# Optimization experiments

Measured on AMD Instinct MI355X. Metric: run time of the kernel, lower is better.

## Reference

```python
import jax, jax.numpy as jnp
import numpy as np

B, N, K = 4, 16384, 8
NF = [8, 32, 64, 128, 256]
E = N * K


def setup_inputs() -> dict:
    key = jax.random.key(0)
    ks = jax.random.split(key, 16)
    x = jax.random.normal(ks[0], (B, N, NF[0]), jnp.float32)
    # knn-style edge list: every node appears as a center K times (no empty segments)
    centers = jnp.tile(jnp.repeat(jnp.arange(N), K)[None, None, :], (B, 1, 1))
    neighbors = jax.random.randint(ks[1], (B, 1, E), 0, N)
    edge_index = jnp.concatenate([centers, neighbors], axis=1)
    specs = [("0a", NF[0], NF[1]), ("0b", NF[0], NF[1]),
             ("1a", NF[1], NF[2]), ("1b", NF[1], NF[2]),
             ("2a", NF[2], NF[3]), ("2b", NF[2], NF[3]),
             ("3a", NF[3], NF[4]), ("3b", NF[3], NF[4]),
             ("cat", NF[1] + NF[2] + NF[3] + NF[4], 1)]
    inp = {"x": x, "edge_index": edge_index}
    for i, (nm, ci, co) in enumerate(specs):
        inp["W" + nm] = jax.random.normal(ks[2 + i], (ci, co), jnp.float32) / np.sqrt(ci)
        inp["g" + nm] = jnp.ones((co,), jnp.float32)   # BN gamma
        inp["b" + nm] = jnp.zeros((co,), jnp.float32)  # BN beta
    inp["bias"] = jnp.zeros((1,), jnp.float32)
    return inp


def _bn(x, g, b):
    # training-mode BatchNorm1d over all rows (GraphBatchNorm1d reduces over batch*num_points)
    m = x.mean(0)
    v = jnp.mean(jnp.square(x - m), 0)  # biased variance, as torch BN uses for normalization
    return g * (x - m) * jax.lax.rsqrt(v + 1e-5) + b


def _mlp(x, W, g, b):
    # Linear(bias=False) -> BN -> LeakyReLU(0.2)
    return jax.nn.leaky_relu(_bn(x @ W, g, b), negative_slope=0.2)


def reference(x, edge_index,
              W0a, g0a, b0a, W0b, g0b, b0b,
              W1a, g1a, b1a, W1b, g1b, b1b,
              W2a, g2a, b2a, W2b, g2b, b2b,
              W3a, g3a, b3a, W3b, g3b, b3b,
              Wcat, gcat, bcat, bias):
    BN = B * N
    xf = x.reshape(BN, NF[0])
    ei = edge_index.transpose(1, 0, 2).reshape(2, -1)  # [2, B*E]
    off = jnp.repeat(jnp.arange(B) * N, E)
    centers = ei[0] + off
    neighbors = ei[1] + off
    segmax = lambda v: jax.ops.segment_max(v, centers, num_segments=BN)
    x0 = _mlp(xf, W0a, g0a, b0a) + segmax(_mlp(xf[neighbors] - xf[centers], W0b, g0b, b0b))
    x1 = _mlp(x0, W1a, g1a, b1a) + segmax(_mlp(x0, W1b, g1b, b1b)[neighbors])
    x2 = _mlp(x1, W2a, g2a, b2a) + segmax(_mlp(x1, W2b, g2b, b2b)[neighbors])
    x3 = _mlp(x2, W3a, g3a, b3a) + segmax(_mlp(x2, W3b, g3b, b3b)[neighbors])
    x_cat = _mlp(jnp.concatenate([x0, x1, x2, x3], axis=-1), Wcat, gcat, bcat)
    return x_cat + bias
```

## Files before the change

kernel.cpp:

```cpp
#include <hip/hip_runtime.h>
#include <math.h>

static constexpr int BB = 4;
static constexpr int NN = 16384;
static constexpr int KK = 8;
static constexpr int EE = 131072;
static constexpr int RR = 65536;
static constexpr int EG = 524288;

static constexpr int SPL = 64;
static constexpr size_t SLOT = (size_t)SPL*512;

static constexpr size_t OFF_X0 = 0;
static constexpr size_t OFF_X1 = OFF_X0 + (size_t)RR*32;
static constexpr size_t OFF_X2 = OFF_X1 + (size_t)RR*64;
static constexpr size_t OFF_X3 = OFF_X2 + (size_t)RR*128;
static constexpr size_t OFF_ZB = OFF_X3 + (size_t)RR*256;
static constexpr size_t OFF_ZC = OFF_ZB + (size_t)RR*128;
static constexpr size_t OFF_S  = OFF_ZC + (size_t)RR;
static constexpr size_t OFF_WP = OFF_S + 9*SLOT;
static constexpr size_t WP1_OFF = 0;
static constexpr size_t WP2_OFF = 4096;
static constexpr size_t WP3_OFF = 4096 + 16384;

__device__ __forceinline__ float lrelu(float x) { return fmaxf(x, 0.2f*x); }

__device__ __forceinline__ unsigned short f2h(float f) {
    _Float16 h = (_Float16)f;
    return *(unsigned short*)&h;
}
__device__ __forceinline__ float h2f(unsigned short u) {
    _Float16 h = *(_Float16*)&u;
    return (float)h;
}

typedef __attribute__((ext_vector_type(8))) _Float16 half8v;
typedef __attribute__((ext_vector_type(8))) unsigned short ushort8v;
typedef __attribute__((ext_vector_type(4))) float float4v;

__global__ __launch_bounds__(256) void k_l0_node(const float* __restrict__ xf,
                                                 const float* __restrict__ W,
                                                 unsigned short* __restrict__ z,
                                                 float* __restrict__ S) {
    __shared__ float w[256];
    __shared__ float red[64];
    int tid = threadIdx.x;
    w[tid] = W[tid];
    if (tid < 64) red[tid] = 0.f;
    __syncthreads();
    int r = blockIdx.x*256 + tid;
    const float4* xr = (const float4*)(xf + (size_t)r*8);
    float4 a = xr[0], b = xr[1];
    float xv[8] = {a.x,a.y,a.z,a.w,b.x,b.y,b.z,b.w};
    float op[32];
#pragma unroll
    for (int c = 0; c < 32; ++c) {
        float s = 0.f;
#pragma unroll
        for (int k = 0; k < 8; ++k) s = fmaf(xv[k], w[k*32+c], s);
        op[c] = s;
    }
    ushort8v* zp = (ushort8v*)(z + (size_t)r*32);
#pragma unroll
    for (int i = 0; i < 4; ++i) {
        ushort8v h;
#pragma unroll
        for (int j = 0; j < 8; ++j) h[j] = f2h(op[i*8+j]);
        zp[i] = h;
    }
#pragma unroll
    for (int c = 0; c < 32; ++c) {
        float s = op[c], q = op[c]*op[c];
#pragma unroll
        for (int off = 32; off >= 1; off >>= 1) {
            s += __shfl_xor(s, off, 64);
            q += __shfl_xor(q, off, 64);
        }
        if ((tid & 63) == 0) { atomicAdd(&red[c], s); atomicAdd(&red[32+c], q); }
    }
    __syncthreads();
    if (tid < 64) atomicAdd(&S[(size_t)(blockIdx.x & (SPL-1))*512 + tid], red[tid]);
}

__global__ __launch_bounds__(256) void k_edge_stats(const float* __restrict__ xf,
                                                    const int* __restrict__ ei,
                                                    const float* __restrict__ W,
                                                    float* __restrict__ S) {
    __shared__ float w[256];
    __shared__ float red[64];
    int tid = threadIdx.x;
    w[tid] = W[tid];
    if (tid < 64) red[tid] = 0.f;
    __syncthreads();
    int g = tid & 3;
    int cg = g*8;
    float s[8], q[8];
#pragma unroll
    for (int j = 0; j < 8; ++j) { s[j] = 0.f; q[j] = 0.f; }
    int qid = (blockIdx.x*256 + tid) >> 2;
    int NQ = (gridDim.x*256) >> 2;
    for (int e = qid; e < EG; e += NQ) {
        int b = e >> 17, jj = e & (EE-1);
        const int* base = ei + (size_t)b*2*EE;
        int ctr = base[jj], nbr = base[EE + jj];
        const float4* pc = (const float4*)(xf + ((size_t)(b<<14) + ctr)*8);
        const float4* pn = (const float4*)(xf + ((size_t)(b<<14) + nbr)*8);
        float4 c0 = pc[0], c1 = pc[1], n0 = pn[0], n1 = pn[1];
        float d[8] = {n0.x-c0.x, n0.y-c0.y, n0.z-c0.z, n0.w-c0.w,
                      n1.x-c1.x, n1.y-c1.y, n1.z-c1.z, n1.w-c1.w};
#pragma unroll
        for (int j = 0; j < 8; ++j) {
            int c = cg + j;
            float z = 0.f;
#pragma unroll
            for (int k = 0; k < 8; ++k) z = fmaf(d[k], w[k*32+c], z);
            s[j] += z; q[j] = fmaf(z, z, q[j]);
        }
    }
#pragma unroll
    for (int off = 4; off <= 32; off <<= 1) {
#pragma unroll
        for (int j = 0; j < 8; ++j) {
            s[j] += __shfl_xor(s[j], off, 64);
            q[j] += __shfl_xor(q[j], off, 64);
        }
    }
    if ((tid & 63) < 4) {
#pragma unroll
        for (int j = 0; j < 8; ++j) {
            atomicAdd(&red[cg + j], s[j]);
            atomicAdd(&red[32 + cg + j], q[j]);
        }
    }
    __syncthreads();
    if (tid < 64) atomicAdd(&S[(size_t)(blockIdx.x & (SPL-1))*512 + tid], red[tid]);
}

__global__ __launch_bounds__(256) void k_edge_apply(const float* __restrict__ xf,
                                                    const int* __restrict__ ei,
                                                    const float* __restrict__ W,
                                                    const float* __restrict__ Sa,
                                                    const float* __restrict__ Sb,
                                                    const float* __restrict__ ga,
                                                    const float* __restrict__ ba,
                                                    const float* __restrict__ gb,
                                                    const float* __restrict__ bbp,
                                                    const float* __restrict__ Wc,
                                                    unsigned short* __restrict__ x0,
                                                    float* __restrict__ zc) {
    __shared__ float w[256];
    __shared__ float scb[32], shb[32], sca[32], sha[32], swc[32];
    int tid = threadIdx.x;
    w[tid] = W[tid];
    if (tid < 32) {
        float su = 0.f, qu = 0.f;
        for (int p = 0; p < SPL; ++p) { su += Sa[(size_t)p*512 + tid]; qu += Sa[(size_t)p*512 + 32 + tid]; }
        float m = su*(1.f/RR);
        float v = fmaxf(qu*(1.f/RR) - m*m, 0.f);
        float sc = ga[tid]*rsqrtf(v + 1e-5f);
        sca[tid] = sc; sha[tid] = fmaf(-m, sc, ba[tid]);
        swc[tid] = Wc[tid];
    } else if (tid < 64) {
        int c = tid - 32;
        float su = 0.f, qu = 0.f;
        for (int p = 0; p < SPL; ++p) { su += Sb[(size_t)p*512 + c]; qu += Sb[(size_t)p*512 + 32 + c]; }
        float m = su*(1.f/EG);
        float v = fmaxf(qu*(1.f/EG) - m*m, 0.f);
        float sc = gb[c]*rsqrtf(v + 1e-5f);
        scb[c] = sc; shb[c] = fmaf(-m, sc, bbp[c]);
    }
    __syncthreads();
    int r = blockIdx.x*256 + tid;
    int b = r >> 14, n = r & (NN-1);
    const int* nb = ei + (size_t)b*2*EE + EE + n*KK;
    const float4* pc = (const float4*)(xf + (size_t)r*8);
    float4 c0 = pc[0], c1 = pc[1];
    float mx[32];
#pragma unroll
    for (int c = 0; c < 32; ++c) mx[c] = -3.0e38f;
    for (int k = 0; k < KK; ++k) {
        int j = nb[k];
        const float4* pn = (const float4*)(xf + ((size_t)(b<<14) + j)*8);
        float4 n0 = pn[0], n1 = pn[1];
        float d[8] = {n0.x-c0.x, n0.y-c0.y, n0.z-c0.z, n0.w-c0.w,
                      n1.x-c1.x, n1.y-c1.y, n1.z-c1.z, n1.w-c1.w};
#pragma unroll
        for (int c = 0; c < 32; ++c) {
            float z = 0.f;
#pragma unroll
            for (int k2 = 0; k2 < 8; ++k2) z = fmaf(d[k2], w[k2*32+c], z);
            float y = lrelu(fmaf(z, scb[c], shb[c]));
            mx[c] = fmaxf(mx[c], y);
        }
    }
    ushort8v* xp = (ushort8v*)(x0 + (size_t)r*32);
    float sdot = 0.f;
#pragma unroll
    for (int i = 0; i < 4; ++i) {
        ushort8v v = xp[i];
        ushort8v o;
#pragma unroll
        for (int j = 0; j < 8; ++j) {
            int c = i*8 + j;
            float val = lrelu(fmaf(h2f(v[j]), sca[c], sha[c])) + mx[c];
            o[j] = f2h(val);
            sdot = fmaf(val, swc[c], sdot);
        }
        xp[i] = o;
    }
    zc[r] = sdot;
}

template<int CI, int CO>
__global__ __launch_bounds__(256) void k_packW(const float* __restrict__ Wa,
                                               const float* __restrict__ Wb,
                                               unsigned short* __restrict__ Wp) {
    constexpr int NT = 2*CO;
    constexpr int KT = CI/32;
    int t = blockIdx.x*256 + threadIdx.x;
    if (t >= NT*CI) return;
    int ng = t % NT, k = t / NT;
    float v = (ng < CO) ? Wa[(size_t)k*CO + ng] : Wb[(size_t)k*CO + (ng - CO)];
    int nt = ng >> 4, n = ng & 15;
    int kt = k >> 5, kq = (k & 31) >> 3, j = k & 7;
    int f = nt*KT + kt;
    int idx = f*512 + ((kq*16 + n)<<3) + j;
    Wp[idx] = f2h(v);
}

template<int CI, int CO>
__global__ __launch_bounds__(256, 3) void k_mfma_dual3(const unsigned short* __restrict__ X,
                                                       const unsigned short* __restrict__ Wp,
                                                       unsigned short* __restrict__ Za,
                                                       unsigned short* __restrict__ Zb,
                                                       float* __restrict__ Sa,
                                                       float* __restrict__ Sb) {
    constexpr int NCH = 4;
    constexpr int KT = CI/32;
    constexpr int WCNT = NCH*KT*512;
    constexpr int ROWT = RR/64;
    constexpr int STR = NCH*16 + 8;
    constexpr int XW  = (CI < 64) ? CI : 64;
    constexpr int PLB = CO/64;
    __shared__ unsigned short Wlds[WCNT];
    __shared__ unsigned short scr[4][16*STR];
    int tid = threadIdx.x;
    int lane = tid & 63, wid = tid >> 6;
    int ch = blockIdx.y;
    int wglob = blockIdx.x*4 + wid;
    int NW = gridDim.x*4;
    int n = lane & 15, kq = lane >> 4;
    int rg = lane >> 3, c8l = (lane & 7)*8;
    unsigned short* myscr = scr[wid];
    size_t pl = (size_t)(wglob & (SPL-1)) * 512;
    bool isA = (ch < PLB);
    unsigned short* Zp = (isA ? Za : Zb) + (size_t)(isA ? ch : ch - PLB)*((size_t)RR*64);
    {
        const ushort8v* src = (const ushort8v*)(Wp + (size_t)ch*WCNT);
        ushort8v* dst = (ushort8v*)Wlds;
        for (int u = tid; u < WCNT/8; u += 256) dst[u] = src[u];
    }
    __syncthreads();

    float4v ps[NCH], pq[NCH];
#pragma unroll
    for (int j = 0; j < NCH; ++j) { ps[j] = (float4v){0,0,0,0}; pq[j] = (float4v){0,0,0,0}; }

    auto issue = [&](half8v (&dst)[4], size_t rowb, int kt) {
        int k0 = kt*32 + kq*8;
        int xpl = k0 >> 6;
        int xoff = k0 & (XW-1);
        const unsigned short* Xp = X + (size_t)xpl*((size_t)RR*64);
#pragma unroll
        for (int i = 0; i < 4; ++i)
            dst[i] = *(const half8v*)&Xp[(rowb + i*16 + n)*XW + xoff];
    };

    auto epilogue = [&](float4v (&acc)[4][NCH], size_t rowbase) {
#pragma unroll
        for (int j = 0; j < NCH; ++j)
#pragma unroll
            for (int i = 0; i < 4; ++i) {
                float4v a4 = acc[i][j];
#pragma unroll
                for (int reg = 0; reg < 4; ++reg) {
                    ps[j][reg] += a4[reg];
                    pq[j][reg] = fmaf(a4[reg], a4[reg], pq[j][reg]);
                }
            }
#pragma unroll
        for (int i = 0; i < 4; ++i) {
            __builtin_amdgcn_wave_barrier();
#pragma unroll
            for (int j = 0; j < NCH; ++j) {
                float4v a4 = acc[i][j];
                ushort4 h = { f2h(a4[0]), f2h(a4[1]), f2h(a4[2]), f2h(a4[3]) };
                *(ushort4*)&myscr[n*STR + j*16 + kq*4] = h;
            }
            __builtin_amdgcn_wave_barrier();
#pragma unroll
            for (int i2 = 0; i2 < 2; ++i2) {
                int rit = rg + i2*8;
                ushort8v v = *(const ushort8v*)&myscr[rit*STR + c8l];
                *(ushort8v*)&Zp[(rowbase + i*16 + rit)*64 + c8l] = v;
            }
        }
    };

    if constexpr (KT == 1) {
        for (int t = wglob; t < ROWT; t += NW) {
            size_t rowbase = (size_t)t*64;
            float4v acc[4][NCH];
#pragma unroll
            for (int i = 0; i < 4; ++i)
#pragma unroll
                for (int j = 0; j < NCH; ++j) acc[i][j] = (float4v){0,0,0,0};
            half8v b[4];
            issue(b, rowbase, 0);
#pragma unroll
            for (int j = 0; j < NCH; ++j) {
                half8v w = *(const half8v*)&Wlds[j*512 + lane*8];
#pragma unroll
                for (int i = 0; i < 4; ++i)
                    acc[i][j] = __builtin_amdgcn_mfma_f32_16x16x32_f16(w, b[i], acc[i][j], 0, 0, 0);
            }
            epilogue(acc, rowbase);
        }
    } else {
        half8v b0[4], b1[4];
        int t = wglob;
        if (t < ROWT) issue(b0, (size_t)t*64, 0);
        for (; t < ROWT; t += NW) {
            size_t rowbase = (size_t)t*64;
            int t2 = t + NW;
            size_t nextrb = (t2 < ROWT) ? (size_t)t2*64 : rowbase;
            float4v acc[4][NCH];
#pragma unroll
            for (int i = 0; i < 4; ++i)
#pragma unroll
                for (int j = 0; j < NCH; ++j) acc[i][j] = (float4v){0,0,0,0};

            auto step = [&](half8v (&bc)[4], half8v (&bn)[4], int kt) {
                if (kt + 1 < KT) issue(bn, rowbase, kt + 1);
                else             issue(bn, nextrb, 0);
#pragma unroll
                for (int j = 0; j < NCH; ++j) {
                    half8v w = *(const half8v*)&Wlds[(j*KT + kt)*512 + lane*8];
#pragma unroll
                    for (int i = 0; i < 4; ++i)
                        acc[i][j] = __builtin_amdgcn_mfma_f32_16x16x32_f16(w, bc[i], acc[i][j], 0, 0, 0);
                }
            };
#pragma unroll
            for (int kh = 0; kh < KT/2; ++kh) {
                step(b0, b1, 2*kh);
                step(b1, b0, 2*kh + 1);
            }
            epilogue(acc, rowbase);
        }
    }

    {
        float* Sg = isA ? Sa : Sb;
        int cb0 = isA ? ch*64 : ch*64 - CO;
#pragma unroll
        for (int j = 0; j < NCH; ++j) {
#pragma unroll
            for (int reg = 0; reg < 4; ++reg) {
                float s = ps[j][reg], q = pq[j][reg];
                s += __shfl_xor(s, 1, 64); q += __shfl_xor(q, 1, 64);
                s += __shfl_xor(s, 2, 64); q += __shfl_xor(q, 2, 64);
                s += __shfl_xor(s, 4, 64); q += __shfl_xor(q, 4, 64);
                s += __shfl_xor(s, 8, 64); q += __shfl_xor(q, 8, 64);
                if (n == 0) {
                    int col = cb0 + j*16 + kq*4 + reg;
                    atomicAdd(&Sg[pl + col], s);
                    atomicAdd(&Sg[pl + CO + col], q);
                }
            }
        }
    }
}

template<int CO>
__global__ __launch_bounds__(256) void k_redstats(float* __restrict__ Sa,
                                                  float* __restrict__ Sb) {
    int t = blockIdx.x*256 + threadIdx.x;
    for (int u = t; u < 2*CO; u += gridDim.x*256) {
        float sa = 0.f, sb = 0.f;
        for (int p = 1; p < SPL; ++p) {
            sa += Sa[(size_t)p*512 + u];
            sb += Sb[(size_t)p*512 + u];
        }
        Sa[u] += sa;
        Sb[u] += sb;
    }
}

template<int CO, bool WRITEBACK>
__global__ __launch_bounds__(256) void k_gathermax(unsigned short* __restrict__ xi,
                                                   const unsigned short* __restrict__ zbh,
                                                   const int* __restrict__ ei,
                                                   const float* __restrict__ Sa,
                                                   const float* __restrict__ Sb,
                                                   const float* __restrict__ ga,
                                                   const float* __restrict__ ba,
                                                   const float* __restrict__ gb,
                                                   const float* __restrict__ bbp,
                                                   const float* __restrict__ Wc,
                                                   int wcoff,
                                                   float* __restrict__ zc) {
    constexpr int CQ = CO/8;
    __shared__ float sca[CO], sha[CO], scb[CO], shb[CO], swc[CO];
    int tid = threadIdx.x;
    for (int u = tid; u < CO; u += 256) {
        float m = Sa[u]*(1.f/RR);
        float v = fmaxf(Sa[CO+u]*(1.f/RR) - m*m, 0.f);
        float sc = ga[u]*rsqrtf(v + 1e-5f);
        sca[u] = sc; sha[u] = fmaf(-m, sc, ba[u]);
        m = Sb[u]*(1.f/RR);
        v = fmaxf(Sb[CO+u]*(1.f/RR) - m*m, 0.f);
        sc = gb[u]*rsqrtf(v + 1e-5f);
        scb[u] = sc; shb[u] = fmaf(-m, sc, bbp[u]);
        swc[u] = Wc[wcoff + u];
    }
    __syncthreads();
    int t = blockIdx.x*256 + tid;
    int r = t / CQ;
    int c8 = (t % CQ)*8;
    int pln = c8 >> 6;
    int off = c8 & 63;
    const unsigned short* zpl = zbh + (size_t)pln*((size_t)RR*64);
    unsigned short* xpl = xi + (size_t)pln*((size_t)RR*64);
    int b = r >> 14, n = r & (NN-1);
    const int* nb = ei + (size_t)b*2*EE + EE + n*KK;
    float sb[8], hb[8];
#pragma unroll
    for (int j = 0; j < 8; ++j) { sb[j] = scb[c8+j]; hb[j] = shb[c8+j]; }
    int nbr[KK];
#pragma unroll
    for (int k = 0; k < KK; ++k) nbr[k] = nb[k];
    size_t bb64 = ((size_t)(b<<14))*64 + off;
    float mx[8];
#pragma unroll
    for (int j = 0; j < 8; ++j) mx[j] = -3e38f;
#pragma unroll
    for (int k = 0; k < KK; ++k) {
        ushort8v u = *(const ushort8v*)(zpl + bb64 + (size_t)nbr[k]*64);
#pragma unroll
        for (int j = 0; j < 8; ++j)
            mx[j] = fmaxf(mx[j], lrelu(fmaf(h2f(u[j]), sb[j], hb[j])));
    }
    ushort8v* xp = (ushort8v*)&xpl[(size_t)r*64 + off];
    ushort8v a = *xp;
    float sdot = 0.f;
    if (WRITEBACK) {
        ushort8v o;
#pragma unroll
        for (int j = 0; j < 8; ++j) {
            float val = lrelu(fmaf(h2f(a[j]), sca[c8+j], sha[c8+j])) + mx[j];
            o[j] = f2h(val);
            sdot = fmaf(val, swc[c8+j], sdot);
        }
        *xp = o;
    } else {
#pragma unroll
        for (int j = 0; j < 8; ++j) {
            float val = lrelu(fmaf(h2f(a[j]), sca[c8+j], sha[c8+j])) + mx[j];
            sdot = fmaf(val, swc[c8+j], sdot);
        }
    }
#pragma unroll
    for (int w = CQ/2; w >= 1; w >>= 1) sdot += __shfl_xor(sdot, w, 64);
    int lane = tid & 63;
    if ((lane & (CQ-1)) == 0) atomicAdd(&zc[r], sdot);
}

__global__ __launch_bounds__(256) void k_catstats(const float* __restrict__ zc,
                                                  float* __restrict__ S8) {
    __shared__ float rs2[2];
    int tid = threadIdx.x;
    if (tid < 2) rs2[tid] = 0.f;
    __syncthreads();
    float v = zc[blockIdx.x*256 + tid];
    float s = v, q = v*v;
#pragma unroll
    for (int off = 32; off >= 1; off >>= 1) {
        s += __shfl_xor(s, off, 64);
        q += __shfl_xor(q, off, 64);
    }
    if ((tid & 63) == 0) { atomicAdd(&rs2[0], s); atomicAdd(&rs2[1], q); }
    __syncthreads();
    if (tid == 0) {
        int p = blockIdx.x & 255;
        atomicAdd(&S8[p*2],     rs2[0]);
        atomicAdd(&S8[p*2 + 1], rs2[1]);
    }
}

__global__ __launch_bounds__(256) void k_catfinal(const float* __restrict__ zc,
                                                  const float* __restrict__ S8,
                                                  const float* __restrict__ g,
                                                  const float* __restrict__ bb,
                                                  const float* __restrict__ bias,
                                                  float* __restrict__ out) {
    __shared__ float rs[256], rq[256];
    int tid = threadIdx.x;
    rs[tid] = S8[tid*2];
    rq[tid] = S8[tid*2 + 1];
    __syncthreads();
#pragma unroll
    for (int h = 128; h >= 1; h >>= 1) {
        if (tid < h) { rs[tid] += rs[tid+h]; rq[tid] += rq[tid+h]; }
        __syncthreads();
    }
    int r = blockIdx.x*256 + tid;
    const float invR = 1.f/65536.f;
    float m = rs[0]*invR;
    float v = fmaxf(rq[0]*invR - m*m, 0.f);
    float sc = g[0]*rsqrtf(v + 1e-5f);
    float sh = fmaf(-m, sc, bb[0]);
    float y = lrelu(fmaf(zc[r], sc, sh));
    out[r] = y + bias[0];
}

extern "C" void kernel_launch(void* const* d_in, const int* in_sizes, int n_in,
                              void* d_out, int out_size, void* d_ws, size_t ws_size,
                              hipStream_t stream) {
    const float* x    = (const float*)d_in[0];
    const int*   ei   = (const int*)d_in[1];
    const float* W0a  = (const float*)d_in[2];
    const float* g0a  = (const float*)d_in[3];
    const float* b0a  = (const float*)d_in[4];
    const float* W0b  = (const float*)d_in[5];
    const float* g0b  = (const float*)d_in[6];
    const float* b0b  = (const float*)d_in[7];
    const float* W1a  = (const float*)d_in[8];
    const float* g1a  = (const float*)d_in[9];
    const float* b1a  = (const float*)d_in[10];
    const float* W1b  = (const float*)d_in[11];
    const float* g1b  = (const float*)d_in[12];
    const float* b1b  = (const float*)d_in[13];
    const float* W2a  = (const float*)d_in[14];
    const float* g2a  = (const float*)d_in[15];
    const float* b2a  = (const float*)d_in[16];
    const float* W2b  = (const float*)d_in[17];
    const float* g2b  = (const float*)d_in[18];
    const float* b2b  = (const float*)d_in[19];
    const float* W3a  = (const float*)d_in[20];
    const float* g3a  = (const float*)d_in[21];
    const float* b3a  = (const float*)d_in[22];
    const float* W3b  = (const float*)d_in[23];
    const float* g3b  = (const float*)d_in[24];
    const float* b3b  = (const float*)d_in[25];
    const float* Wcat = (const float*)d_in[26];
    const float* gcat = (const float*)d_in[27];
    const float* bcat = (const float*)d_in[28];
    const float* bias = (const float*)d_in[29];
    float* out = (float*)d_out;

    float* ws = (float*)d_ws;
    unsigned short* x0 = (unsigned short*)(ws + OFF_X0);
    unsigned short* x1 = (unsigned short*)(ws + OFF_X1);
    unsigned short* x2 = (unsigned short*)(ws + OFF_X2);
    unsigned short* x3 = (unsigned short*)(ws + OFF_X3);
    unsigned short* zbh = (unsigned short*)(ws + OFF_ZB);
    float* zc = ws + OFF_ZC;
    float* S  = ws + OFF_S;
    unsigned short* wpbase = (unsigned short*)(ws + OFF_WP);
    unsigned short* wp1 = wpbase + WP1_OFF;
    unsigned short* wp2 = wpbase + WP2_OFF;
    unsigned short* wp3 = wpbase + WP3_OFF;
    auto Sl = [&](int i) { return S + (size_t)i*SLOT; };

    hipMemsetAsync(S, 0, 9*SLOT*sizeof(float), stream);

    k_packW<32,64><<<(128*32+255)/256, 256, 0, stream>>>(W1a, W1b, wp1);
    k_packW<64,128><<<(256*64+255)/256, 256, 0, stream>>>(W2a, W2b, wp2);
    k_packW<128,256><<<(512*128+255)/256, 256, 0, stream>>>(W3a, W3b, wp3);

    k_l0_node<<<RR/256, 256, 0, stream>>>(x, W0a, x0, Sl(0));
    k_edge_stats<<<512, 256, 0, stream>>>(x, ei, W0b, Sl(1));
    k_edge_apply<<<RR/256, 256, 0, stream>>>(x, ei, W0b, Sl(0), Sl(1),
                                             g0a, b0a, g0b, b0b, Wcat, x0, zc);

    k_mfma_dual3<32,64><<<dim3(256,2), 256, 0, stream>>>(x0, wp1, x1, zbh, Sl(2), Sl(3));
    k_redstats<64><<<4, 256, 0, stream>>>(Sl(2), Sl(3));
    k_gathermax<64,true><<<RR*8/256, 256, 0, stream>>>(x1, zbh, ei, Sl(2), Sl(3),
                                                       g1a, b1a, g1b, b1b, Wcat, 32, zc);

    k_mfma_dual3<64,128><<<dim3(192,4), 256, 0, stream>>>(x1, wp2, x2, zbh, Sl(4), Sl(5));
    k_redstats<128><<<4, 256, 0, stream>>>(Sl(4), Sl(5));
    k_gathermax<128,true><<<RR*16/256, 256, 0, stream>>>(x2, zbh, ei, Sl(4), Sl(5),
                                                         g2a, b2a, g2b, b2b, Wcat, 96, zc);

    k_mfma_dual3<128,256><<<dim3(96,8), 256, 0, stream>>>(x2, wp3, x3, zbh, Sl(6), Sl(7));
    k_redstats<256><<<4, 256, 0, stream>>>(Sl(6), Sl(7));
    k_gathermax<256,false><<<RR*32/256, 256, 0, stream>>>(x3, zbh, ei, Sl(6), Sl(7),
                                                          g3a, b3a, g3b, b3b, Wcat, 224, zc);

    k_catstats<<<RR/256, 256, 0, stream>>>(zc, Sl(8));
    k_catfinal<<<RR/256, 256, 0, stream>>>(zc, Sl(8), gcat, bcat, bias, out);
}
```

Measured before the change: 310.7 us.

## Hoist BN+LeakyReLU out of segment max, keep weights in registers, fuse prep kernels

Several changes land together. The BN affine and LeakyReLU are pulled out of the per-neighbor max by taking a sign-adjusted max first and applying a monotone transform once, since scaling by |sc| followed by LeakyReLU is monotone. The MFMA kernel holds packed weights in registers instead of LDS, and its grid sizes and occupancy bounds change. The memset and three weight-pack launches are merged into one prep kernel. Gathermax issues all neighbor loads up front with vectorized index loads and a swizzled block order. The costs are higher register pressure, which may spill for CI=128 with KT=4, and the prep kernel zeroing S with a grid-stride loop.

```diff
diff --git a/kernel.cpp b/kernel.cpp
--- a/kernel.cpp
+++ b/kernel.cpp
@@ -149,7 +149,7 @@
                                                     unsigned short* __restrict__ x0,
                                                     float* __restrict__ zc) {
     __shared__ float w[256];
-    __shared__ float scb[32], shb[32], sca[32], sha[32], swc[32];
+    __shared__ float scbA[32], sgnb[32], shb[32], sca[32], sha[32], swc[32];
     int tid = threadIdx.x;
     w[tid] = W[tid];
     if (tid < 32) {
@@ -167,19 +167,22 @@
         float m = su*(1.f/EG);
         float v = fmaxf(qu*(1.f/EG) - m*m, 0.f);
         float sc = gb[c]*rsqrtf(v + 1e-5f);
-        scb[c] = sc; shb[c] = fmaf(-m, sc, bbp[c]);
+        scbA[c] = fabsf(sc); sgnb[c] = (sc >= 0.f) ? 1.f : -1.f;
+        shb[c] = fmaf(-m, sc, bbp[c]);
     }
     __syncthreads();
     int r = blockIdx.x*256 + tid;
     int b = r >> 14, n = r & (NN-1);
-    const int* nb = ei + (size_t)b*2*EE + EE + n*KK;
+    const int4* nb4 = (const int4*)(ei + (size_t)b*2*EE + EE + n*KK);
+    int4 q0 = nb4[0], q1 = nb4[1];
+    int nbr[KK] = {q0.x,q0.y,q0.z,q0.w,q1.x,q1.y,q1.z,q1.w};
     const float4* pc = (const float4*)(xf + (size_t)r*8);
     float4 c0 = pc[0], c1 = pc[1];
     float mx[32];
 #pragma unroll
     for (int c = 0; c < 32; ++c) mx[c] = -3.0e38f;
     for (int k = 0; k < KK; ++k) {
-        int j = nb[k];
+        int j = nbr[k];
         const float4* pn = (const float4*)(xf + ((size_t)(b<<14) + j)*8);
         float4 n0 = pn[0], n1 = pn[1];
         float d[8] = {n0.x-c0.x, n0.y-c0.y, n0.z-c0.z, n0.w-c0.w,
@@ -189,8 +192,7 @@
             float z = 0.f;
 #pragma unroll
             for (int k2 = 0; k2 < 8; ++k2) z = fmaf(d[k2], w[k2*32+c], z);
-            float y = lrelu(fmaf(z, scb[c], shb[c]));
-            mx[c] = fmaxf(mx[c], y);
+            mx[c] = fmaxf(mx[c], sgnb[c]*z);
         }
     }
     ushort8v* xp = (ushort8v*)(x0 + (size_t)r*32);
@@ -202,7 +204,8 @@
 #pragma unroll
         for (int j = 0; j < 8; ++j) {
             int c = i*8 + j;
-            float val = lrelu(fmaf(h2f(v[j]), sca[c], sha[c])) + mx[c];
+            float y = lrelu(fmaf(mx[c], scbA[c], shb[c]));
+            float val = lrelu(fmaf(h2f(v[j]), sca[c], sha[c])) + y;
             o[j] = f2h(val);
             sdot = fmaf(val, swc[c], sdot);
         }
@@ -212,13 +215,11 @@
 }
 
 template<int CI, int CO>
-__global__ __launch_bounds__(256) void k_packW(const float* __restrict__ Wa,
-                                               const float* __restrict__ Wb,
-                                               unsigned short* __restrict__ Wp) {
+__device__ __forceinline__ void packone(int t, const float* __restrict__ Wa,
+                                        const float* __restrict__ Wb,
+                                        unsigned short* __restrict__ Wp) {
     constexpr int NT = 2*CO;
     constexpr int KT = CI/32;
-    int t = blockIdx.x*256 + threadIdx.x;
-    if (t >= NT*CI) return;
     int ng = t % NT, k = t / NT;
     float v = (ng < CO) ? Wa[(size_t)k*CO + ng] : Wb[(size_t)k*CO + (ng - CO)];
     int nt = ng >> 4, n = ng & 15;
@@ -228,13 +229,28 @@
     Wp[idx] = f2h(v);
 }
 
-template<int CI, int CO>
-__global__ __launch_bounds__(256, 3) void k_mfma_dual3(const unsigned short* __restrict__ X,
-                                                       const unsigned short* __restrict__ Wp,
-                                                       unsigned short* __restrict__ Za,
-                                                       unsigned short* __restrict__ Zb,
-                                                       float* __restrict__ Sa,
-                                                       float* __restrict__ Sb) {
+__global__ __launch_bounds__(256) void k_prep(const float* __restrict__ W1a, const float* __restrict__ W1b,
+                                              const float* __restrict__ W2a, const float* __restrict__ W2b,
+                                              const float* __restrict__ W3a, const float* __restrict__ W3b,
+                                              unsigned short* __restrict__ wp1,
+                                              unsigned short* __restrict__ wp2,
+                                              unsigned short* __restrict__ wp3,
+                                              float* __restrict__ S) {
+    int t = blockIdx.x*256 + threadIdx.x;
+    int NT_ = gridDim.x*256;
+    for (int u = t; u < (int)(9*SLOT); u += NT_) S[u] = 0.f;
+    for (int u = t; u < 32*128;  u += NT_) packone<32,64>(u, W1a, W1b, wp1);
+    for (int u = t; u < 64*256;  u += NT_) packone<64,128>(u, W2a, W2b, wp2);
+    for (int u = t; u < 128*512; u += NT_) packone<128,256>(u, W3a, W3b, wp3);
+}
+
+template<int CI, int CO, int MW>
+__global__ __launch_bounds__(256, MW) void k_mfma_dual4(const unsigned short* __restrict__ X,
+                                                        const unsigned short* __restrict__ Wp,
+                                                        unsigned short* __restrict__ Za,
+                                                        unsigned short* __restrict__ Zb,
+                                                        float* __restrict__ Sa,
+                                                        float* __restrict__ Sb) {
     constexpr int NCH = 4;
     constexpr int KT = CI/32;
     constexpr int WCNT = NCH*KT*512;
@@ -242,7 +258,6 @@
     constexpr int STR = NCH*16 + 8;
     constexpr int XW  = (CI < 64) ? CI : 64;
     constexpr int PLB = CO/64;
-    __shared__ unsigned short Wlds[WCNT];
     __shared__ unsigned short scr[4][16*STR];
     int tid = threadIdx.x;
     int lane = tid & 63, wid = tid >> 6;
@@ -255,12 +270,16 @@
     size_t pl = (size_t)(wglob & (SPL-1)) * 512;
     bool isA = (ch < PLB);
     unsigned short* Zp = (isA ? Za : Zb) + (size_t)(isA ? ch : ch - PLB)*((size_t)RR*64);
+
+    half8v wreg[KT][NCH];
     {
-        const ushort8v* src = (const ushort8v*)(Wp + (size_t)ch*WCNT);
-        ushort8v* dst = (ushort8v*)Wlds;
-        for (int u = tid; u < WCNT/8; u += 256) dst[u] = src[u];
-    }
-    __syncthreads();
+        const unsigned short* Wc = Wp + (size_t)ch*WCNT;
+#pragma unroll
+        for (int kt = 0; kt < KT; ++kt)
+#pragma unroll
+            for (int j = 0; j < NCH; ++j)
+                wreg[kt][j] = *(const half8v*)&Wc[(j*KT + kt)*512 + lane*8];
+    }
 
     float4v ps[NCH], pq[NCH];
 #pragma unroll
@@ -318,12 +337,10 @@
             half8v b[4];
             issue(b, rowbase, 0);
 #pragma unroll
-            for (int j = 0; j < NCH; ++j) {
-                half8v w = *(const half8v*)&Wlds[j*512 + lane*8];
+            for (int j = 0; j < NCH; ++j)
 #pragma unroll
                 for (int i = 0; i < 4; ++i)
-                    acc[i][j] = __builtin_amdgcn_mfma_f32_16x16x32_f16(w, b[i], acc[i][j], 0, 0, 0);
-            }
+                    acc[i][j] = __builtin_amdgcn_mfma_f32_16x16x32_f16(wreg[0][j], b[i], acc[i][j], 0, 0, 0);
             epilogue(acc, rowbase);
         }
     } else {
@@ -344,12 +361,10 @@
                 if (kt + 1 < KT) issue(bn, rowbase, kt + 1);
                 else             issue(bn, nextrb, 0);
 #pragma unroll
-                for (int j = 0; j < NCH; ++j) {
-                    half8v w = *(const half8v*)&Wlds[(j*KT + kt)*512 + lane*8];
+                for (int j = 0; j < NCH; ++j)
 #pragma unroll
                     for (int i = 0; i < 4; ++i)
-                        acc[i][j] = __builtin_amdgcn_mfma_f32_16x16x32_f16(w, bc[i], acc[i][j], 0, 0, 0);
-                }
+                        acc[i][j] = __builtin_amdgcn_mfma_f32_16x16x32_f16(wreg[kt][j], bc[i], acc[i][j], 0, 0, 0);
             };
 #pragma unroll
             for (int kh = 0; kh < KT/2; ++kh) {
@@ -411,7 +426,7 @@
                                                    int wcoff,
                                                    float* __restrict__ zc) {
     constexpr int CQ = CO/8;
-    __shared__ float sca[CO], sha[CO], scb[CO], shb[CO], swc[CO];
+    __shared__ float sca[CO], sha[CO], sbA[CO], shb[CO], swc[CO], sgn[CO];
     int tid = threadIdx.x;
     for (int u = tid; u < CO; u += 256) {
         float m = Sa[u]*(1.f/RR);
@@ -421,11 +436,13 @@
         m = Sb[u]*(1.f/RR);
         v = fmaxf(Sb[CO+u]*(1.f/RR) - m*m, 0.f);
         sc = gb[u]*rsqrtf(v + 1e-5f);
-        scb[u] = sc; shb[u] = fmaf(-m, sc, bbp[u]);
+        sbA[u] = fabsf(sc); sgn[u] = (sc >= 0.f) ? 1.f : -1.f;
+        shb[u] = fmaf(-m, sc, bbp[u]);
         swc[u] = Wc[wcoff + u];
     }
     __syncthreads();
-    int t = blockIdx.x*256 + tid;
+    int bx = (int)((blockIdx.x & 7)*(gridDim.x >> 3) + (blockIdx.x >> 3));
+    int t = bx*256 + tid;
     int r = t / CQ;
     int c8 = (t % CQ)*8;
     int pln = c8 >> 6;
@@ -433,41 +450,46 @@
     const unsigned short* zpl = zbh + (size_t)pln*((size_t)RR*64);
     unsigned short* xpl = xi + (size_t)pln*((size_t)RR*64);
     int b = r >> 14, n = r & (NN-1);
-    const int* nb = ei + (size_t)b*2*EE + EE + n*KK;
-    float sb[8], hb[8];
-#pragma unroll
-    for (int j = 0; j < 8; ++j) { sb[j] = scb[c8+j]; hb[j] = shb[c8+j]; }
-    int nbr[KK];
-#pragma unroll
-    for (int k = 0; k < KK; ++k) nbr[k] = nb[k];
+    const int4* nb4 = (const int4*)(ei + (size_t)b*2*EE + EE + n*KK);
+    int4 q0 = nb4[0], q1 = nb4[1];
+    int nbr[KK] = {q0.x,q0.y,q0.z,q0.w,q1.x,q1.y,q1.z,q1.w};
     size_t bb64 = ((size_t)(b<<14))*64 + off;
-    float mx[8];
-#pragma unroll
-    for (int j = 0; j < 8; ++j) mx[j] = -3e38f;
-#pragma unroll
-    for (int k = 0; k < KK; ++k) {
-        ushort8v u = *(const ushort8v*)(zpl + bb64 + (size_t)nbr[k]*64);
-#pragma unroll
-        for (int j = 0; j < 8; ++j)
-            mx[j] = fmaxf(mx[j], lrelu(fmaf(h2f(u[j]), sb[j], hb[j])));
-    }
     ushort8v* xp = (ushort8v*)&xpl[(size_t)r*64 + off];
     ushort8v a = *xp;
+    ushort8v u[KK];
+#pragma unroll
+    for (int k = 0; k < KK; ++k)
+        u[k] = *(const ushort8v*)(zpl + bb64 + (size_t)nbr[k]*64);
+    float sg[8], sb[8], hb[8];
+#pragma unroll
+    for (int j = 0; j < 8; ++j) { sg[j] = sgn[c8+j]; sb[j] = sbA[c8+j]; hb[j] = shb[c8+j]; }
+    float mx[8];
+#pragma unroll
+    for (int j = 0; j < 8; ++j) mx[j] = -3e38f;
+#pragma unroll
+    for (int k = 0; k < KK; ++k)
+#pragma unroll
+        for (int j = 0; j < 8; ++j)
+            mx[j] = fmaxf(mx[j], sg[j]*h2f(u[k][j]));
     float sdot = 0.f;
     if (WRITEBACK) {
         ushort8v o;
 #pragma unroll
         for (int j = 0; j < 8; ++j) {
-            float val = lrelu(fmaf(h2f(a[j]), sca[c8+j], sha[c8+j])) + mx[j];
+            int c = c8 + j;
+            float y = lrelu(fmaf(mx[j], sb[j], hb[j]));
+            float val = lrelu(fmaf(h2f(a[j]), sca[c], sha[c])) + y;
             o[j] = f2h(val);
-            sdot = fmaf(val, swc[c8+j], sdot);
+            sdot = fmaf(val, swc[c], sdot);
         }
         *xp = o;
     } else {
 #pragma unroll
         for (int j = 0; j < 8; ++j) {
-            float val = lrelu(fmaf(h2f(a[j]), sca[c8+j], sha[c8+j])) + mx[j];
-            sdot = fmaf(val, swc[c8+j], sdot);
+            int c = c8 + j;
+            float y = lrelu(fmaf(mx[j], sb[j], hb[j]));
+            float val = lrelu(fmaf(h2f(a[j]), sca[c], sha[c])) + y;
+            sdot = fmaf(val, swc[c], sdot);
         }
     }
 #pragma unroll
@@ -573,28 +595,24 @@
     unsigned short* wp3 = wpbase + WP3_OFF;
     auto Sl = [&](int i) { return S + (size_t)i*SLOT; };
 
-    hipMemsetAsync(S, 0, 9*SLOT*sizeof(float), stream);
-
-    k_packW<32,64><<<(128*32+255)/256, 256, 0, stream>>>(W1a, W1b, wp1);
-    k_packW<64,128><<<(256*64+255)/256, 256, 0, stream>>>(W2a, W2b, wp2);
-    k_packW<128,256><<<(512*128+255)/256, 256, 0, stream>>>(W3a, W3b, wp3);
+    k_prep<<<256, 256, 0, stream>>>(W1a, W1b, W2a, W2b, W3a, W3b, wp1, wp2, wp3, S);
 
     k_l0_node<<<RR/256, 256, 0, stream>>>(x, W0a, x0, Sl(0));
     k_edge_stats<<<512, 256, 0, stream>>>(x, ei, W0b, Sl(1));
     k_edge_apply<<<RR/256, 256, 0, stream>>>(x, ei, W0b, Sl(0), Sl(1),
                                              g0a, b0a, g0b, b0b, Wcat, x0, zc);
 
-    k_mfma_dual3<32,64><<<dim3(256,2), 256, 0, stream>>>(x0, wp1, x1, zbh, Sl(2), Sl(3));
+    k_mfma_dual4<32,64,3><<<dim3(256,2), 256, 0, stream>>>(x0, wp1, x1, zbh, Sl(2), Sl(3));
     k_redstats<64><<<4, 256, 0, stream>>>(Sl(2), Sl(3));
     k_gathermax<64,true><<<RR*8/256, 256, 0, stream>>>(x1, zbh, ei, Sl(2), Sl(3),
                                                        g1a, b1a, g1b, b1b, Wcat, 32, zc);
 
-    k_mfma_dual3<64,128><<<dim3(192,4), 256, 0, stream>>>(x1, wp2, x2, zbh, Sl(4), Sl(5));
+    k_mfma_dual4<64,128,3><<<dim3(128,4), 256, 0, stream>>>(x1, wp2, x2, zbh, Sl(4), Sl(5));
     k_redstats<128><<<4, 256, 0, stream>>>(Sl(4), Sl(5));
     k_gathermax<128,true><<<RR*16/256, 256, 0, stream>>>(x2, zbh, ei, Sl(4), Sl(5),
                                                          g2a, b2a, g2b, b2b, Wcat, 96, zc);
 
-    k_mfma_dual3<128,256><<<dim3(96,8), 256, 0, stream>>>(x2, wp3, x3, zbh, Sl(6), Sl(7));
+    k_mfma_dual4<128,256,2><<<dim3(64,8), 256, 0, stream>>>(x2, wp3, x3, zbh, Sl(6), Sl(7));
     k_redstats<256><<<4, 256, 0, stream>>>(Sl(6), Sl(7));
     k_gathermax<256,false><<<RR*32/256, 256, 0, stream>>>(x3, zbh, ei, Sl(6), Sl(7),
                                                           g3a, b3a, g3b, b3b, Wcat, 224, zc);
```

Measured after the change: 298.1 us. -4.1%, faster.
